# Kernel tuning notes

Measured on AMD Instinct MI355X. Metric: run time of the kernel, lower is better.

## Reference

```python
import jax, jax.numpy as jnp
import numpy as np

B, T, I, H, L, O = 256, 256, 128, 512, 2, 1


def _lstm_layer(x_tbi, W_ih, W_hh, b_ih, b_hh):
    # x_tbi: [T, B, in_dim]; returns full output sequence [T, B, H]
    # Precompute input projections for all timesteps at once (big GEMM).
    x_proj = jnp.einsum('tbi,gi->tbg', x_tbi, W_ih) + b_ih + b_hh  # [T, B, 4H]
    h0 = jnp.zeros((x_tbi.shape[1], H), x_tbi.dtype)
    c0 = jnp.zeros_like(h0)

    def step(carry, xp):
        h, c = carry
        gates = xp + h @ W_hh.T  # [B, 4H]
        i_g, f_g, g_g, o_g = jnp.split(gates, 4, axis=-1)  # torch order: i,f,g,o
        i_g = jax.nn.sigmoid(i_g)
        f_g = jax.nn.sigmoid(f_g)
        g_g = jnp.tanh(g_g)
        o_g = jax.nn.sigmoid(o_g)
        c_new = f_g * c + i_g * g_g
        h_new = o_g * jnp.tanh(c_new)
        return (h_new, c_new), h_new

    (_, _), hs = jax.lax.scan(step, (h0, c0), x_proj)
    return hs  # [T, B, H]


def setup_inputs() -> dict:
    key = jax.random.key(0)
    ks = jax.random.split(key, 11)
    s_ih0 = 1.0 / np.sqrt(H)
    inp = {
        'x': jax.random.normal(ks[0], (B, T, I), jnp.float32),
        'W_ih0': jax.random.uniform(ks[1], (4 * H, I), jnp.float32, -s_ih0, s_ih0),
        'W_hh0': jax.random.uniform(ks[2], (4 * H, H), jnp.float32, -s_ih0, s_ih0),
        'b_ih0': jax.random.uniform(ks[3], (4 * H,), jnp.float32, -s_ih0, s_ih0),
        'b_hh0': jax.random.uniform(ks[4], (4 * H,), jnp.float32, -s_ih0, s_ih0),
        'W_ih1': jax.random.uniform(ks[5], (4 * H, H), jnp.float32, -s_ih0, s_ih0),
        'W_hh1': jax.random.uniform(ks[6], (4 * H, H), jnp.float32, -s_ih0, s_ih0),
        'b_ih1': jax.random.uniform(ks[7], (4 * H,), jnp.float32, -s_ih0, s_ih0),
        'b_hh1': jax.random.uniform(ks[8], (4 * H,), jnp.float32, -s_ih0, s_ih0),
        'fc_w': jax.random.uniform(ks[9], (O, H), jnp.float32, -s_ih0, s_ih0),
        'fc_b': jax.random.uniform(ks[10], (O,), jnp.float32, -s_ih0, s_ih0),
    }
    return inp


def reference(x, W_ih0, W_hh0, b_ih0, b_hh0, W_ih1, W_hh1, b_ih1, b_hh1, fc_w, fc_b):
    x_tbi = jnp.transpose(x, (1, 0, 2))  # [T, B, I]
    h1 = _lstm_layer(x_tbi, W_ih0, W_hh0, b_ih0, b_hh0)  # [T, B, H]
    h2 = _lstm_layer(h1, W_ih1, W_hh1, b_ih1, b_hh1)     # [T, B, H]
    last = h2[-1]                                         # [B, H] == out[:, -1, :]
    return last @ fc_w.T + fc_b                           # [B, O]
```

## Files before the change

### kernel.cpp

```cpp
#include <hip/hip_runtime.h>
#include <stdint.h>

typedef _Float16 f16;
typedef _Float16 f16x8 __attribute__((ext_vector_type(8)));
typedef float f32x4 __attribute__((ext_vector_type(4)));

#define TT 256
#define BB 256
#define II 128
#define HH 512
#define G4 2048
#define NGRP 8
static constexpr size_t BH = (size_t)BB * HH;

__device__ __forceinline__ uint64_t ld_agent_u64(const uint64_t* p) {
  return __hip_atomic_load(p, __ATOMIC_RELAXED, __HIP_MEMORY_SCOPE_AGENT);
}
__device__ __forceinline__ void st_agent_u64(uint64_t* p, uint64_t v) {
  __hip_atomic_store(p, v, __ATOMIC_RELAXED, __HIP_MEMORY_SCOPE_AGENT);
}
__device__ __forceinline__ void st_agent_u16(uint16_t* p, uint16_t v) {
  __hip_atomic_store(p, v, __ATOMIC_RELAXED, __HIP_MEMORY_SCOPE_AGENT);
}
__device__ __forceinline__ uint4 mk4(uint64_t a, uint64_t b) {
  uint4 r;
  r.x = (uint32_t)a; r.y = (uint32_t)(a >> 32);
  r.z = (uint32_t)b; r.w = (uint32_t)(b >> 32);
  return r;
}

__device__ __forceinline__ float fsig(float x) {
  x = fminf(fmaxf(x, -30.f), 30.f);
  float e = __builtin_amdgcn_exp2f(-1.44269504f * x);
  return __builtin_amdgcn_rcpf(1.f + e);
}
__device__ __forceinline__ float ftanh(float x) {
  x = fminf(fmaxf(x, -15.f), 15.f);
  float e = __builtin_amdgcn_exp2f(-2.88539008f * x);
  return (1.f - e) * __builtin_amdgcn_rcpf(1.f + e);
}

__device__ __forceinline__ f16x8 ldfragh(const f16* S, int row, int gi) {
  return *(const f16x8*)(S + row * 512 + ((gi ^ (row & 7)) * 8));
}
__device__ __forceinline__ f16x8 ldfragx(const f16* S, int row, int gi) {
  return *(const f16x8*)(S + row * 128 + ((gi ^ (row & 7)) * 8));
}

__global__ void k_diag(float* out, float val) { out[0] = val; }

__global__ __launch_bounds__(256) void k_conv_x(const float* __restrict__ x,
                                                f16* __restrict__ xt) {
  int idx = blockIdx.x * 256 + threadIdx.x;
  int row = idx >> 4;
  int ii = (idx & 15) * 8;
  int t = row >> 8, b = row & 255;
  const float4* xs = (const float4*)(x + ((size_t)b * TT + t) * II + ii);
  float4 v0 = xs[0];
  float4 v1 = xs[1];
  f16x8 h;
  h[0] = (f16)v0.x; h[1] = (f16)v0.y; h[2] = (f16)v0.z; h[3] = (f16)v0.w;
  h[4] = (f16)v1.x; h[5] = (f16)v1.y; h[6] = (f16)v1.z; h[7] = (f16)v1.w;
  *(f16x8*)(xt + (size_t)row * II + ii) = h;
}

__global__ __launch_bounds__(256) void k_conv_w(
    const float* __restrict__ wih0, const float* __restrict__ whh0,
    const float* __restrict__ wih1, const float* __restrict__ whh1,
    const float* __restrict__ bih0, const float* __restrict__ bhh0,
    const float* __restrict__ bih1, const float* __restrict__ bhh1,
    f16* owih0, f16* owhh0, f16* owih1, f16* owhh1, float* ob0, float* ob1) {
  int i = blockIdx.x * 256 + threadIdx.x;
  if (i < G4 * II) owih0[i] = (f16)wih0[i];
  if (i < G4 * HH) {
    owhh0[i] = (f16)whh0[i];
    owih1[i] = (f16)wih1[i];
    owhh1[i] = (f16)whh1[i];
  }
  if (i < G4) {
    ob0[i] = bih0[i] + bhh0[i];
    ob1[i] = bih1[i] + bhh1[i];
  }
}

__global__ __launch_bounds__(256, 1) void k_fused(
    const f16* __restrict__ xt,
    const f16* __restrict__ Wih0, const f16* __restrict__ Whh0,
    const f16* __restrict__ Wih1, const f16* __restrict__ Whh1,
    const float* __restrict__ b0, const float* __restrict__ b1,
    f16* __restrict__ h1r, f16* __restrict__ h2r, uint16_t* __restrict__ flags) {
  __shared__ __align__(16) f16 h1s[32 * 512];
  __shared__ __align__(16) f16 h2s[32 * 512];
  __shared__ __align__(16) f16 xs[32 * 128];
  __shared__ __align__(16) float gs[2][64][36];

  int tid = threadIdx.x;
  int l64 = tid & 63;
  int wid = tid >> 6;
  int lm = l64 & 15, ls = l64 >> 4;
  int bx = blockIdx.x;
  int grp = bx & 7;
  int slice = bx >> 3;
  int col0 = slice * 16;
  int row0 = grp * 32;

  int wrow = wid * 512 + col0 + lm;
  f16x8 wih0f[4], whh0f[16], wih1f[16], whh1f[16];
#pragma unroll
  for (int kk = 0; kk < 4; ++kk)
    wih0f[kk] = *(const f16x8*)(Wih0 + (size_t)wrow * II + kk * 32 + ls * 8);
#pragma unroll
  for (int kk = 0; kk < 16; ++kk) {
    whh0f[kk] = *(const f16x8*)(Whh0 + (size_t)wrow * HH + kk * 32 + ls * 8);
    wih1f[kk] = *(const f16x8*)(Wih1 + (size_t)wrow * HH + kk * 32 + ls * 8);
    whh1f[kk] = *(const f16x8*)(Whh1 + (size_t)wrow * HH + kk * 32 + ls * 8);
  }

  int el = tid >> 7;
  int er = (tid >> 2) & 31;
  int eq = tid & 3;
  const float* bsrc = el ? b1 : b0;
  float bias[4][4];
#pragma unroll
  for (int g = 0; g < 4; ++g)
#pragma unroll
    for (int j = 0; j < 4; ++j) bias[g][j] = bsrc[g * HH + col0 + eq * 4 + j];
  float cst[4] = {0.f, 0.f, 0.f, 0.f};
  f16* ering = el ? h2r : h1r;

  int sr = tid >> 3;
  int gx = tid & 7;
  const uint64_t kTarget = 0x0001000100010001ULL;

#pragma unroll 1
  for (int u = 0; u <= TT; ++u) {
    uint4 xv0, xv1;
    if (u < TT) {
      const uint4* src = (const uint4*)(xt + ((size_t)u * BB + row0 + sr) * II);
      xv0 = src[gx];
      xv1 = src[gx + 8];
    }
    if (u > 0) {
      const uint64_t* fl =
          (const uint64_t*)(flags + ((size_t)grp * (TT + 1) + (u - 1)) * 32);
      int guard = 0;
      for (;;) {
        uint64_t v = ld_agent_u64(fl + (l64 & 3));
        if (__all(v == kTarget)) break;
        if (++guard > 200000) break;
        __builtin_amdgcn_s_sleep(1);
      }
      asm volatile("" ::: "memory");
      const uint64_t* s1 = (const uint64_t*)(h1r + (size_t)((u - 1) & 1) * BH +
                                             (size_t)(row0 + sr) * HH);
      uint64_t va[16], vb[16];
#pragma unroll
      for (int q = 0; q < 8; ++q) {
        int gi = gx + q * 8;
        va[2 * q]     = ld_agent_u64(s1 + gi * 2);
        va[2 * q + 1] = ld_agent_u64(s1 + gi * 2 + 1);
      }
      if (u >= 2) {
        const uint64_t* s2 = (const uint64_t*)(h2r + (size_t)(u & 1) * BH +
                                               (size_t)(row0 + sr) * HH);
#pragma unroll
        for (int q = 0; q < 8; ++q) {
          int gi = gx + q * 8;
          vb[2 * q]     = ld_agent_u64(s2 + gi * 2);
          vb[2 * q + 1] = ld_agent_u64(s2 + gi * 2 + 1);
        }
      }
      uint4* d1 = (uint4*)h1s;
#pragma unroll
      for (int q = 0; q < 8; ++q) {
        int gi = gx + q * 8;
        d1[sr * 64 + (gi ^ (sr & 7))] = mk4(va[2 * q], va[2 * q + 1]);
      }
      if (u >= 2) {
        uint4* d2 = (uint4*)h2s;
#pragma unroll
        for (int q = 0; q < 8; ++q) {
          int gi = gx + q * 8;
          d2[sr * 64 + (gi ^ (sr & 7))] = mk4(vb[2 * q], vb[2 * q + 1]);
        }
      }
    }
    if (u < TT) {
      uint4* dx = (uint4*)xs;
      dx[sr * 16 + (gx ^ (sr & 7))] = xv0;
      dx[sr * 16 + ((gx + 8) ^ (sr & 7))] = xv1;
    }
    __syncthreads();

    f32x4 a0f0 = {0.f, 0.f, 0.f, 0.f}, a0f1 = {0.f, 0.f, 0.f, 0.f};
    f32x4 a1f0 = {0.f, 0.f, 0.f, 0.f}, a1f1 = {0.f, 0.f, 0.f, 0.f};
    if (u < TT) {
#pragma unroll
      for (int kk = 0; kk < 4; ++kk) {
        f16x8 xA = ldfragx(xs, lm, kk * 4 + ls);
        f16x8 xB = ldfragx(xs, 16 + lm, kk * 4 + ls);
        a0f0 = __builtin_amdgcn_mfma_f32_16x16x32_f16(xA, wih0f[kk], a0f0, 0, 0, 0);
        a0f1 = __builtin_amdgcn_mfma_f32_16x16x32_f16(xB, wih0f[kk], a0f1, 0, 0, 0);
      }
    }
    if (u > 0) {
#pragma unroll
      for (int kk = 0; kk < 16; ++kk) {
        f16x8 hA = ldfragh(h1s, lm, kk * 4 + ls);
        f16x8 hB = ldfragh(h1s, 16 + lm, kk * 4 + ls);
        if (u < TT) {
          a0f0 = __builtin_amdgcn_mfma_f32_16x16x32_f16(hA, whh0f[kk], a0f0, 0, 0, 0);
          a0f1 = __builtin_amdgcn_mfma_f32_16x16x32_f16(hB, whh0f[kk], a0f1, 0, 0, 0);
        }
        a1f0 = __builtin_amdgcn_mfma_f32_16x16x32_f16(hA, wih1f[kk], a1f0, 0, 0, 0);
        a1f1 = __builtin_amdgcn_mfma_f32_16x16x32_f16(hB, wih1f[kk], a1f1, 0, 0, 0);
      }
      if (u >= 2) {
#pragma unroll
        for (int kk = 0; kk < 16; ++kk) {
          f16x8 hA = ldfragh(h2s, lm, kk * 4 + ls);
          f16x8 hB = ldfragh(h2s, 16 + lm, kk * 4 + ls);
          a1f0 = __builtin_amdgcn_mfma_f32_16x16x32_f16(hA, whh1f[kk], a1f0, 0, 0, 0);
          a1f1 = __builtin_amdgcn_mfma_f32_16x16x32_f16(hB, whh1f[kk], a1f1, 0, 0, 0);
        }
      }
    }
    *(f32x4*)&gs[0][wid * 16 + lm][ls * 4] = a0f0;
    *(f32x4*)&gs[0][wid * 16 + lm][16 + ls * 4] = a0f1;
    *(f32x4*)&gs[1][wid * 16 + lm][ls * 4] = a1f0;
    *(f32x4*)&gs[1][wid * 16 + lm][16 + ls * 4] = a1f1;
    __syncthreads();

    bool act = el ? (u >= 1) : (u < TT);
    if (act) {
      int t_l = el ? (u - 1) : u;
      int slot = t_l & 1;
      union { uint64_t v; unsigned short us[4]; } pk;
#pragma unroll
      for (int j = 0; j < 4; ++j) {
        int cl = eq * 4 + j;
        float pi = gs[el][0 * 16 + cl][er] + bias[0][j];
        float pf = gs[el][1 * 16 + cl][er] + bias[1][j];
        float pg = gs[el][2 * 16 + cl][er] + bias[2][j];
        float po = gs[el][3 * 16 + cl][er] + bias[3][j];
        float ig = fsig(pi), fg = fsig(pf), gg = ftanh(pg), og = fsig(po);
        cst[j] = fg * cst[j] + ig * gg;
        pk.us[j] = __builtin_bit_cast(unsigned short, (f16)(og * ftanh(cst[j])));
      }
      uint64_t* dst = (uint64_t*)(ering + (size_t)slot * BH +
                                  (size_t)(row0 + er) * HH + col0 + eq * 4);
      st_agent_u64(dst, pk.v);
    }
    asm volatile("s_waitcnt vmcnt(0)" ::: "memory");
    __syncthreads();
    if (u < TT && tid == 0)
      st_agent_u16(flags + ((size_t)grp * (TT + 1) + u) * 32 + slice, 1u);
  }
}

__global__ __launch_bounds__(64) void k_fc(const f16* __restrict__ h2,
                                           const float* __restrict__ fcw,
                                           const float* __restrict__ fcb,
                                           float* __restrict__ out) {
  int b = blockIdx.x;
  int l = threadIdx.x;
  f16x8 hv = *(const f16x8*)(h2 + (size_t)b * HH + l * 8);
  float4 w0 = ((const float4*)fcw)[l * 2];
  float4 w1 = ((const float4*)fcw)[l * 2 + 1];
  float s = (float)hv[0] * w0.x + (float)hv[1] * w0.y + (float)hv[2] * w0.z +
            (float)hv[3] * w0.w + (float)hv[4] * w1.x + (float)hv[5] * w1.y +
            (float)hv[6] * w1.z + (float)hv[7] * w1.w;
#pragma unroll
  for (int off = 32; off > 0; off >>= 1) s += __shfl_down(s, off);
  if (l == 0) out[b] = s + fcb[0];
}

extern "C" void kernel_launch(void* const* d_in, const int* in_sizes, int n_in,
                              void* d_out, int out_size, void* d_ws, size_t ws_size,
                              hipStream_t stream) {
  (void)in_sizes; (void)n_in; (void)out_size;

  const float* x    = (const float*)d_in[0];
  const float* wih0 = (const float*)d_in[1];
  const float* whh0 = (const float*)d_in[2];
  const float* bih0 = (const float*)d_in[3];
  const float* bhh0 = (const float*)d_in[4];
  const float* wih1 = (const float*)d_in[5];
  const float* whh1 = (const float*)d_in[6];
  const float* bih1 = (const float*)d_in[7];
  const float* bhh1 = (const float*)d_in[8];
  const float* fcw  = (const float*)d_in[9];
  const float* fcb  = (const float*)d_in[10];

  const size_t SZ_XT   = (size_t)TT * BB * II * 2;
  const size_t SZ_WIH0 = (size_t)G4 * II * 2;
  const size_t SZ_W    = (size_t)G4 * HH * 2;
  const size_t SZ_B    = (size_t)G4 * 4;
  const size_t SZ_RING = (size_t)2 * BH * 2;
  const size_t SZ_FLG  = (size_t)NGRP * (TT + 1) * 64;
  const size_t TOTAL = SZ_XT + SZ_WIH0 + 3 * SZ_W + 2 * SZ_B + 2 * SZ_RING + SZ_FLG;

  if (ws_size < TOTAL) {
    k_diag<<<1, 1, 0, stream>>>((float*)d_out, (float)(ws_size >> 20));
    return;
  }

  char* ws = (char*)d_ws;
  size_t off = 0;
  f16* xt    = (f16*)(ws + off); off += SZ_XT;
  f16* cwih0 = (f16*)(ws + off); off += SZ_WIH0;
  f16* cwhh0 = (f16*)(ws + off); off += SZ_W;
  f16* cwih1 = (f16*)(ws + off); off += SZ_W;
  f16* cwhh1 = (f16*)(ws + off); off += SZ_W;
  float* b0  = (float*)(ws + off); off += SZ_B;
  float* b1  = (float*)(ws + off); off += SZ_B;
  f16* h1r   = (f16*)(ws + off); off += SZ_RING;
  f16* h2r   = (f16*)(ws + off); off += SZ_RING;
  uint16_t* flags = (uint16_t*)(ws + off); off += SZ_FLG;

  hipMemsetAsync(flags, 0, SZ_FLG, stream);
  k_conv_w<<<4096, 256, 0, stream>>>(wih0, whh0, wih1, whh1, bih0, bhh0, bih1, bhh1,
                                     cwih0, cwhh0, cwih1, cwhh1, b0, b1);
  k_conv_x<<<4096, 256, 0, stream>>>(x, xt);
  k_fused<<<256, 256, 0, stream>>>(xt, cwih0, cwhh0, cwih1, cwhh1, b0, b1,
                                   h1r, h2r, flags);
  k_fc<<<256, 64, 0, stream>>>(h2r + BH, fcw, fcb, (float*)d_out);
}
```

Before: 1.559 ms.

## Halve persistent block count with 512-thread blocks covering 32 hidden columns each

The fused persistent LSTM kernel now launches 128 blocks of 512 threads instead of 256 blocks of 256. Each block covers 32 hidden columns with two waves per gate, which halves the number of blocks that must signal and poll flags every timestep. The h-state ring reload now uses inline-asm dwordx4 loads with the sc1 cache bit instead of 64-bit agent-scope atomic loads. Biases are staged in shared memory rather than held in registers. In exchange, per-step elementwise work per block doubles and more threads wait at each barrier, and the sc1 loads depend on that bit giving coherent reads of data written by other blocks.

```diff
diff --git a/kernel.cpp b/kernel.cpp
--- a/kernel.cpp
+++ b/kernel.cpp
@@ -11,6 +11,7 @@
 #define HH 512
 #define G4 2048
 #define NGRP 8
+#define NSLC 16
 static constexpr size_t BH = (size_t)BB * HH;
 
 __device__ __forceinline__ uint64_t ld_agent_u64(const uint64_t* p) {
@@ -22,11 +23,21 @@
 __device__ __forceinline__ void st_agent_u16(uint16_t* p, uint16_t v) {
   __hip_atomic_store(p, v, __ATOMIC_RELAXED, __HIP_MEMORY_SCOPE_AGENT);
 }
-__device__ __forceinline__ uint4 mk4(uint64_t a, uint64_t b) {
-  uint4 r;
-  r.x = (uint32_t)a; r.y = (uint32_t)(a >> 32);
-  r.z = (uint32_t)b; r.w = (uint32_t)(b >> 32);
-  return r;
+__device__ __forceinline__ void ld8_sc1(const void* b1, const void* b2, uint4 v[8]) {
+  asm volatile(
+      "global_load_dwordx4 %0, %8, off sc1\n\t"
+      "global_load_dwordx4 %1, %8, off offset:256 sc1\n\t"
+      "global_load_dwordx4 %2, %8, off offset:512 sc1\n\t"
+      "global_load_dwordx4 %3, %8, off offset:768 sc1\n\t"
+      "global_load_dwordx4 %4, %9, off sc1\n\t"
+      "global_load_dwordx4 %5, %9, off offset:256 sc1\n\t"
+      "global_load_dwordx4 %6, %9, off offset:512 sc1\n\t"
+      "global_load_dwordx4 %7, %9, off offset:768 sc1\n\t"
+      "s_waitcnt vmcnt(4)"
+      : "=&v"(v[0]), "=&v"(v[1]), "=&v"(v[2]), "=&v"(v[3]),
+        "=&v"(v[4]), "=&v"(v[5]), "=&v"(v[6]), "=&v"(v[7])
+      : "v"(b1), "v"(b2)
+      : "memory");
 }
 
 __device__ __forceinline__ float fsig(float x) {
@@ -83,7 +94,7 @@
   }
 }
 
-__global__ __launch_bounds__(256, 1) void k_fused(
+__global__ __launch_bounds__(512, 2) void k_fused(
     const f16* __restrict__ xt,
     const f16* __restrict__ Wih0, const f16* __restrict__ Whh0,
     const f16* __restrict__ Wih1, const f16* __restrict__ Whh1,
@@ -92,19 +103,28 @@
   __shared__ __align__(16) f16 h1s[32 * 512];
   __shared__ __align__(16) f16 h2s[32 * 512];
   __shared__ __align__(16) f16 xs[32 * 128];
-  __shared__ __align__(16) float gs[2][64][36];
+  __shared__ __align__(16) float gs[2][128][36];
+  __shared__ float bl[2][4][32];
 
   int tid = threadIdx.x;
   int l64 = tid & 63;
   int wid = tid >> 6;
+  int g = wid >> 1;
+  int ch = wid & 1;
   int lm = l64 & 15, ls = l64 >> 4;
   int bx = blockIdx.x;
   int grp = bx & 7;
   int slice = bx >> 3;
-  int col0 = slice * 16;
+  int col0 = slice * 32;
   int row0 = grp * 32;
 
-  int wrow = wid * 512 + col0 + lm;
+  if (tid < 256) {
+    int el_ = tid >> 7, gt = (tid >> 5) & 3, cl = tid & 31;
+    const float* bsrc = el_ ? b1 : b0;
+    bl[el_][gt][cl] = bsrc[gt * HH + col0 + cl];
+  }
+
+  int wrow = g * 512 + col0 + ch * 16 + lm;
   f16x8 wih0f[4], whh0f[16], wih1f[16], whh1f[16];
 #pragma unroll
   for (int kk = 0; kk < 4; ++kk)
@@ -116,79 +136,55 @@
     whh1f[kk] = *(const f16x8*)(Whh1 + (size_t)wrow * HH + kk * 32 + ls * 8);
   }
 
-  int el = tid >> 7;
-  int er = (tid >> 2) & 31;
-  int eq = tid & 3;
-  const float* bsrc = el ? b1 : b0;
-  float bias[4][4];
-#pragma unroll
-  for (int g = 0; g < 4; ++g)
-#pragma unroll
-    for (int j = 0; j < 4; ++j) bias[g][j] = bsrc[g * HH + col0 + eq * 4 + j];
+  int el = tid >> 8;
+  int er = (tid >> 3) & 31;
+  int eq = tid & 7;
   float cst[4] = {0.f, 0.f, 0.f, 0.f};
   f16* ering = el ? h2r : h1r;
 
-  int sr = tid >> 3;
-  int gx = tid & 7;
+  int sr = tid >> 4;
+  int gq = tid & 15;
   const uint64_t kTarget = 0x0001000100010001ULL;
+  __syncthreads();
 
 #pragma unroll 1
   for (int u = 0; u <= TT; ++u) {
-    uint4 xv0, xv1;
-    if (u < TT) {
-      const uint4* src = (const uint4*)(xt + ((size_t)u * BB + row0 + sr) * II);
-      xv0 = src[gx];
-      xv1 = src[gx + 8];
-    }
+    uint4 xv;
+    if (u < TT)
+      xv = ((const uint4*)(xt + ((size_t)u * BB + row0 + sr) * II))[gq];
     if (u > 0) {
       const uint64_t* fl =
           (const uint64_t*)(flags + ((size_t)grp * (TT + 1) + (u - 1)) * 32);
       int guard = 0;
       for (;;) {
-        uint64_t v = ld_agent_u64(fl + (l64 & 3));
+        uint64_t v = ld_agent_u64(fl + (l64 & 1));
         if (__all(v == kTarget)) break;
-        if (++guard > 200000) break;
+        if (++guard > 500000) break;
         __builtin_amdgcn_s_sleep(1);
       }
       asm volatile("" ::: "memory");
-      const uint64_t* s1 = (const uint64_t*)(h1r + (size_t)((u - 1) & 1) * BH +
-                                             (size_t)(row0 + sr) * HH);
-      uint64_t va[16], vb[16];
-#pragma unroll
-      for (int q = 0; q < 8; ++q) {
-        int gi = gx + q * 8;
-        va[2 * q]     = ld_agent_u64(s1 + gi * 2);
-        va[2 * q + 1] = ld_agent_u64(s1 + gi * 2 + 1);
-      }
-      if (u >= 2) {
-        const uint64_t* s2 = (const uint64_t*)(h2r + (size_t)(u & 1) * BH +
-                                               (size_t)(row0 + sr) * HH);
-#pragma unroll
-        for (int q = 0; q < 8; ++q) {
-          int gi = gx + q * 8;
-          vb[2 * q]     = ld_agent_u64(s2 + gi * 2);
-          vb[2 * q + 1] = ld_agent_u64(s2 + gi * 2 + 1);
-        }
-      }
+      const f16* base1 =
+          h1r + (size_t)((u - 1) & 1) * BH + (size_t)(row0 + sr) * HH + gq * 8;
+      const f16* base2 =
+          h2r + (size_t)(u & 1) * BH + (size_t)(row0 + sr) * HH + gq * 8;
+      uint4 v[8];
+      ld8_sc1(base1, base2, v);
       uint4* d1 = (uint4*)h1s;
-#pragma unroll
-      for (int q = 0; q < 8; ++q) {
-        int gi = gx + q * 8;
-        d1[sr * 64 + (gi ^ (sr & 7))] = mk4(va[2 * q], va[2 * q + 1]);
-      }
-      if (u >= 2) {
-        uint4* d2 = (uint4*)h2s;
-#pragma unroll
-        for (int q = 0; q < 8; ++q) {
-          int gi = gx + q * 8;
-          d2[sr * 64 + (gi ^ (sr & 7))] = mk4(vb[2 * q], vb[2 * q + 1]);
-        }
+      uint4* d2 = (uint4*)h2s;
+#pragma unroll
+      for (int q = 0; q < 4; ++q) {
+        int gi = gq + q * 16;
+        d1[sr * 64 + (gi ^ (sr & 7))] = v[q];
+      }
+      asm volatile("s_waitcnt vmcnt(0)" ::: "memory");
+#pragma unroll
+      for (int q = 0; q < 4; ++q) {
+        int gi = gq + q * 16;
+        d2[sr * 64 + (gi ^ (sr & 7))] = v[4 + q];
       }
     }
     if (u < TT) {
-      uint4* dx = (uint4*)xs;
-      dx[sr * 16 + (gx ^ (sr & 7))] = xv0;
-      dx[sr * 16 + ((gx + 8) ^ (sr & 7))] = xv1;
+      ((uint4*)xs)[sr * 16 + (gq ^ (sr & 7))] = xv;
     }
     __syncthreads();
 
@@ -225,10 +221,11 @@
         }
       }
     }
-    *(f32x4*)&gs[0][wid * 16 + lm][ls * 4] = a0f0;
-    *(f32x4*)&gs[0][wid * 16 + lm][16 + ls * 4] = a0f1;
-    *(f32x4*)&gs[1][wid * 16 + lm][ls * 4] = a1f0;
-    *(f32x4*)&gs[1][wid * 16 + lm][16 + ls * 4] = a1f1;
+    int gl = g * 32 + ch * 16 + lm;
+    *(f32x4*)&gs[0][gl][ls * 4] = a0f0;
+    *(f32x4*)&gs[0][gl][16 + ls * 4] = a0f1;
+    *(f32x4*)&gs[1][gl][ls * 4] = a1f0;
+    *(f32x4*)&gs[1][gl][16 + ls * 4] = a1f1;
     __syncthreads();
 
     bool act = el ? (u >= 1) : (u < TT);
@@ -239,10 +236,10 @@
 #pragma unroll
       for (int j = 0; j < 4; ++j) {
         int cl = eq * 4 + j;
-        float pi = gs[el][0 * 16 + cl][er] + bias[0][j];
-        float pf = gs[el][1 * 16 + cl][er] + bias[1][j];
-        float pg = gs[el][2 * 16 + cl][er] + bias[2][j];
-        float po = gs[el][3 * 16 + cl][er] + bias[3][j];
+        float pi = gs[el][0 * 32 + cl][er] + bl[el][0][cl];
+        float pf = gs[el][1 * 32 + cl][er] + bl[el][1][cl];
+        float pg = gs[el][2 * 32 + cl][er] + bl[el][2][cl];
+        float po = gs[el][3 * 32 + cl][er] + bl[el][3][cl];
         float ig = fsig(pi), fg = fsig(pf), gg = ftanh(pg), og = fsig(po);
         cst[j] = fg * cst[j] + ig * gg;
         pk.us[j] = __builtin_bit_cast(unsigned short, (f16)(og * ftanh(cst[j])));
@@ -298,7 +295,8 @@
   const size_t SZ_B    = (size_t)G4 * 4;
   const size_t SZ_RING = (size_t)2 * BH * 2;
   const size_t SZ_FLG  = (size_t)NGRP * (TT + 1) * 64;
-  const size_t TOTAL = SZ_XT + SZ_WIH0 + 3 * SZ_W + 2 * SZ_B + 2 * SZ_RING + SZ_FLG;
+  const size_t TOTAL =
+      SZ_XT + SZ_WIH0 + 3 * SZ_W + 2 * SZ_B + 2 * SZ_RING + SZ_FLG;
 
   if (ws_size < TOTAL) {
     k_diag<<<1, 1, 0, stream>>>((float*)d_out, (float)(ws_size >> 20));
@@ -322,7 +320,7 @@
   k_conv_w<<<4096, 256, 0, stream>>>(wih0, whh0, wih1, whh1, bih0, bhh0, bih1, bhh1,
                                      cwih0, cwhh0, cwih1, cwhh1, b0, b1);
   k_conv_x<<<4096, 256, 0, stream>>>(x, xt);
-  k_fused<<<256, 256, 0, stream>>>(xt, cwih0, cwhh0, cwih1, cwhh1, b0, b1,
+  k_fused<<<128, 512, 0, stream>>>(xt, cwih0, cwhh0, cwih1, cwhh1, b0, b1,
                                    h1r, h2r, flags);
   k_fc<<<256, 64, 0, stream>>>(h2r + BH, fcw, fcb, (float*)d_out);
 }
```

Result: slower. 1.866 ms (+19.7%).

## Split per-layer flags and publish layer-0 h before layer-1 GEMM

Applied to the files above, without the earlier changes.

Gives each layer its own flag array and per-wave flag lanes, so layer-0 hidden state is computed, stored and signalled right after the layer-0 GEMM, before the layer-1 GEMM runs. This moves layer 0 off the critical path of layer 1 and lets other blocks start the next step earlier. The h1/h2 ring reads become one batch of inline-asm dwordx4 loads with the sc1 cache bit, and the h2 LDS write is deferred until after the layer-0 MFMAs. This adds an extra barrier per step, hand-written waitcnt logic, and a wait on both layers' flags.

```diff
diff --git a/kernel.cpp b/kernel.cpp
--- a/kernel.cpp
+++ b/kernel.cpp
@@ -12,6 +12,8 @@
 #define G4 2048
 #define NGRP 8
 static constexpr size_t BH = (size_t)BB * HH;
+static constexpr size_t FLG_LINE_U16 = 64;
+static constexpr size_t FLG_LAYER_OFF = (size_t)NGRP * (TT + 1) * FLG_LINE_U16;
 
 __device__ __forceinline__ uint64_t ld_agent_u64(const uint64_t* p) {
   return __hip_atomic_load(p, __ATOMIC_RELAXED, __HIP_MEMORY_SCOPE_AGENT);
@@ -22,11 +24,31 @@
 __device__ __forceinline__ void st_agent_u16(uint16_t* p, uint16_t v) {
   __hip_atomic_store(p, v, __ATOMIC_RELAXED, __HIP_MEMORY_SCOPE_AGENT);
 }
-__device__ __forceinline__ uint4 mk4(uint64_t a, uint64_t b) {
-  uint4 r;
-  r.x = (uint32_t)a; r.y = (uint32_t)(a >> 32);
-  r.z = (uint32_t)b; r.w = (uint32_t)(b >> 32);
-  return r;
+__device__ __forceinline__ void ld16_sc1(const void* b1, const void* b2, uint4 v[16]) {
+  asm volatile(
+      "global_load_dwordx4 %0, %16, off sc1\n\t"
+      "global_load_dwordx4 %1, %16, off offset:128 sc1\n\t"
+      "global_load_dwordx4 %2, %16, off offset:256 sc1\n\t"
+      "global_load_dwordx4 %3, %16, off offset:384 sc1\n\t"
+      "global_load_dwordx4 %4, %16, off offset:512 sc1\n\t"
+      "global_load_dwordx4 %5, %16, off offset:640 sc1\n\t"
+      "global_load_dwordx4 %6, %16, off offset:768 sc1\n\t"
+      "global_load_dwordx4 %7, %16, off offset:896 sc1\n\t"
+      "global_load_dwordx4 %8, %17, off sc1\n\t"
+      "global_load_dwordx4 %9, %17, off offset:128 sc1\n\t"
+      "global_load_dwordx4 %10, %17, off offset:256 sc1\n\t"
+      "global_load_dwordx4 %11, %17, off offset:384 sc1\n\t"
+      "global_load_dwordx4 %12, %17, off offset:512 sc1\n\t"
+      "global_load_dwordx4 %13, %17, off offset:640 sc1\n\t"
+      "global_load_dwordx4 %14, %17, off offset:768 sc1\n\t"
+      "global_load_dwordx4 %15, %17, off offset:896 sc1\n\t"
+      "s_waitcnt vmcnt(8)"
+      : "=&v"(v[0]), "=&v"(v[1]), "=&v"(v[2]), "=&v"(v[3]),
+        "=&v"(v[4]), "=&v"(v[5]), "=&v"(v[6]), "=&v"(v[7]),
+        "=&v"(v[8]), "=&v"(v[9]), "=&v"(v[10]), "=&v"(v[11]),
+        "=&v"(v[12]), "=&v"(v[13]), "=&v"(v[14]), "=&v"(v[15])
+      : "v"(b1), "v"(b2)
+      : "memory");
 }
 
 __device__ __forceinline__ float fsig(float x) {
@@ -140,49 +162,41 @@
       xv0 = src[gx];
       xv1 = src[gx + 8];
     }
+    uint4 hv[16];
     if (u > 0) {
-      const uint64_t* fl =
-          (const uint64_t*)(flags + ((size_t)grp * (TT + 1) + (u - 1)) * 32);
+      const uint64_t* fl1 =
+          (const uint64_t*)(flags + ((size_t)grp * (TT + 1) + (u - 1)) * FLG_LINE_U16);
+      const uint64_t* fl2 =
+          (const uint64_t*)(flags + FLG_LAYER_OFF +
+                            ((size_t)grp * (TT + 1) + (u >= 2 ? u - 2 : 0)) * FLG_LINE_U16);
       int guard = 0;
-      for (;;) {
-        uint64_t v = ld_agent_u64(fl + (l64 & 3));
-        if (__all(v == kTarget)) break;
-        if (++guard > 200000) break;
-        __builtin_amdgcn_s_sleep(1);
+      if (u >= 2) {
+        for (;;) {
+          uint64_t v1 = ld_agent_u64(fl1 + (l64 & 7));
+          uint64_t v2 = ld_agent_u64(fl2 + (l64 & 7));
+          if (__all((v1 == kTarget) && (v2 == kTarget))) break;
+          if (++guard > 500000) break;
+          __builtin_amdgcn_s_sleep(1);
+        }
+      } else {
+        for (;;) {
+          uint64_t v1 = ld_agent_u64(fl1 + (l64 & 7));
+          if (__all(v1 == kTarget)) break;
+          if (++guard > 500000) break;
+          __builtin_amdgcn_s_sleep(1);
+        }
       }
       asm volatile("" ::: "memory");
-      const uint64_t* s1 = (const uint64_t*)(h1r + (size_t)((u - 1) & 1) * BH +
-                                             (size_t)(row0 + sr) * HH);
-      uint64_t va[16], vb[16];
+      const f16* base1 =
+          h1r + (size_t)((u - 1) & 1) * BH + (size_t)(row0 + sr) * HH + gx * 8;
+      const f16* base2 =
+          h2r + (size_t)(u & 1) * BH + (size_t)(row0 + sr) * HH + gx * 8;
+      ld16_sc1(base1, base2, hv);
+      uint4* d1 = (uint4*)h1s;
 #pragma unroll
       for (int q = 0; q < 8; ++q) {
         int gi = gx + q * 8;
-        va[2 * q]     = ld_agent_u64(s1 + gi * 2);
-        va[2 * q + 1] = ld_agent_u64(s1 + gi * 2 + 1);
-      }
-      if (u >= 2) {
-        const uint64_t* s2 = (const uint64_t*)(h2r + (size_t)(u & 1) * BH +
-                                               (size_t)(row0 + sr) * HH);
-#pragma unroll
-        for (int q = 0; q < 8; ++q) {
-          int gi = gx + q * 8;
-          vb[2 * q]     = ld_agent_u64(s2 + gi * 2);
-          vb[2 * q + 1] = ld_agent_u64(s2 + gi * 2 + 1);
-        }
-      }
-      uint4* d1 = (uint4*)h1s;
-#pragma unroll
-      for (int q = 0; q < 8; ++q) {
-        int gi = gx + q * 8;
-        d1[sr * 64 + (gi ^ (sr & 7))] = mk4(va[2 * q], va[2 * q + 1]);
-      }
-      if (u >= 2) {
-        uint4* d2 = (uint4*)h2s;
-#pragma unroll
-        for (int q = 0; q < 8; ++q) {
-          int gi = gx + q * 8;
-          d2[sr * 64 + (gi ^ (sr & 7))] = mk4(vb[2 * q], vb[2 * q + 1]);
-        }
+        d1[sr * 64 + (gi ^ (sr & 7))] = hv[q];
       }
     }
     if (u < TT) {
@@ -192,9 +206,8 @@
     }
     __syncthreads();
 
-    f32x4 a0f0 = {0.f, 0.f, 0.f, 0.f}, a0f1 = {0.f, 0.f, 0.f, 0.f};
-    f32x4 a1f0 = {0.f, 0.f, 0.f, 0.f}, a1f1 = {0.f, 0.f, 0.f, 0.f};
     if (u < TT) {
+      f32x4 a0f0 = {0.f, 0.f, 0.f, 0.f}, a0f1 = {0.f, 0.f, 0.f, 0.f};
 #pragma unroll
       for (int kk = 0; kk < 4; ++kk) {
         f16x8 xA = ldfragx(xs, lm, kk * 4 + ls);
@@ -202,16 +215,58 @@
         a0f0 = __builtin_amdgcn_mfma_f32_16x16x32_f16(xA, wih0f[kk], a0f0, 0, 0, 0);
         a0f1 = __builtin_amdgcn_mfma_f32_16x16x32_f16(xB, wih0f[kk], a0f1, 0, 0, 0);
       }
+      if (u > 0) {
+#pragma unroll
+        for (int kk = 0; kk < 16; ++kk) {
+          f16x8 hA = ldfragh(h1s, lm, kk * 4 + ls);
+          f16x8 hB = ldfragh(h1s, 16 + lm, kk * 4 + ls);
+          a0f0 = __builtin_amdgcn_mfma_f32_16x16x32_f16(hA, whh0f[kk], a0f0, 0, 0, 0);
+          a0f1 = __builtin_amdgcn_mfma_f32_16x16x32_f16(hB, whh0f[kk], a0f1, 0, 0, 0);
+        }
+      }
+      *(f32x4*)&gs[0][wid * 16 + lm][ls * 4] = a0f0;
+      *(f32x4*)&gs[0][wid * 16 + lm][16 + ls * 4] = a0f1;
     }
     if (u > 0) {
+      asm volatile("s_waitcnt vmcnt(0)" ::: "memory");
+      uint4* d2 = (uint4*)h2s;
+#pragma unroll
+      for (int q = 0; q < 8; ++q) {
+        int gi = gx + q * 8;
+        d2[sr * 64 + (gi ^ (sr & 7))] = hv[8 + q];
+      }
+    }
+    __syncthreads();
+
+    if (u < TT && wid < 2) {
+      union { uint64_t v; unsigned short us[4]; } pk;
+#pragma unroll
+      for (int j = 0; j < 4; ++j) {
+        int cl = eq * 4 + j;
+        float pi = gs[0][0 * 16 + cl][er] + bias[0][j];
+        float pf = gs[0][1 * 16 + cl][er] + bias[1][j];
+        float pg = gs[0][2 * 16 + cl][er] + bias[2][j];
+        float po = gs[0][3 * 16 + cl][er] + bias[3][j];
+        float ig = fsig(pi), fg = fsig(pf), gg = ftanh(pg), og = fsig(po);
+        cst[j] = fg * cst[j] + ig * gg;
+        pk.us[j] = __builtin_bit_cast(unsigned short, (f16)(og * ftanh(cst[j])));
+      }
+      st_agent_u64((uint64_t*)(h1r + (size_t)(u & 1) * BH +
+                               (size_t)(row0 + er) * HH + col0 + eq * 4),
+                   pk.v);
+      asm volatile("s_waitcnt vmcnt(0)" ::: "memory");
+      if (l64 == 0)
+        st_agent_u16(flags + ((size_t)grp * (TT + 1) + u) * FLG_LINE_U16 +
+                         slice * 2 + wid,
+                     1u);
+    }
+
+    if (u > 0) {
+      f32x4 a1f0 = {0.f, 0.f, 0.f, 0.f}, a1f1 = {0.f, 0.f, 0.f, 0.f};
 #pragma unroll
       for (int kk = 0; kk < 16; ++kk) {
         f16x8 hA = ldfragh(h1s, lm, kk * 4 + ls);
         f16x8 hB = ldfragh(h1s, 16 + lm, kk * 4 + ls);
-        if (u < TT) {
-          a0f0 = __builtin_amdgcn_mfma_f32_16x16x32_f16(hA, whh0f[kk], a0f0, 0, 0, 0);
-          a0f1 = __builtin_amdgcn_mfma_f32_16x16x32_f16(hB, whh0f[kk], a0f1, 0, 0, 0);
-        }
         a1f0 = __builtin_amdgcn_mfma_f32_16x16x32_f16(hA, wih1f[kk], a1f0, 0, 0, 0);
         a1f1 = __builtin_amdgcn_mfma_f32_16x16x32_f16(hB, wih1f[kk], a1f1, 0, 0, 0);
       }
@@ -224,37 +279,34 @@
           a1f1 = __builtin_amdgcn_mfma_f32_16x16x32_f16(hB, whh1f[kk], a1f1, 0, 0, 0);
         }
       }
-    }
-    *(f32x4*)&gs[0][wid * 16 + lm][ls * 4] = a0f0;
-    *(f32x4*)&gs[0][wid * 16 + lm][16 + ls * 4] = a0f1;
-    *(f32x4*)&gs[1][wid * 16 + lm][ls * 4] = a1f0;
-    *(f32x4*)&gs[1][wid * 16 + lm][16 + ls * 4] = a1f1;
+      *(f32x4*)&gs[1][wid * 16 + lm][ls * 4] = a1f0;
+      *(f32x4*)&gs[1][wid * 16 + lm][16 + ls * 4] = a1f1;
+    }
     __syncthreads();
 
-    bool act = el ? (u >= 1) : (u < TT);
-    if (act) {
-      int t_l = el ? (u - 1) : u;
-      int slot = t_l & 1;
+    if (u > 0 && wid >= 2) {
       union { uint64_t v; unsigned short us[4]; } pk;
 #pragma unroll
       for (int j = 0; j < 4; ++j) {
         int cl = eq * 4 + j;
-        float pi = gs[el][0 * 16 + cl][er] + bias[0][j];
-        float pf = gs[el][1 * 16 + cl][er] + bias[1][j];
-        float pg = gs[el][2 * 16 + cl][er] + bias[2][j];
-        float po = gs[el][3 * 16 + cl][er] + bias[3][j];
+        float pi = gs[1][0 * 16 + cl][er] + bias[0][j];
+        float pf = gs[1][1 * 16 + cl][er] + bias[1][j];
+        float pg = gs[1][2 * 16 + cl][er] + bias[2][j];
+        float po = gs[1][3 * 16 + cl][er] + bias[3][j];
         float ig = fsig(pi), fg = fsig(pf), gg = ftanh(pg), og = fsig(po);
         cst[j] = fg * cst[j] + ig * gg;
         pk.us[j] = __builtin_bit_cast(unsigned short, (f16)(og * ftanh(cst[j])));
       }
-      uint64_t* dst = (uint64_t*)(ering + (size_t)slot * BH +
-                                  (size_t)(row0 + er) * HH + col0 + eq * 4);
-      st_agent_u64(dst, pk.v);
-    }
-    asm volatile("s_waitcnt vmcnt(0)" ::: "memory");
-    __syncthreads();
-    if (u < TT && tid == 0)
-      st_agent_u16(flags + ((size_t)grp * (TT + 1) + u) * 32 + slice, 1u);
+      st_agent_u64((uint64_t*)(h2r + (size_t)((u - 1) & 1) * BH +
+                               (size_t)(row0 + er) * HH + col0 + eq * 4),
+                   pk.v);
+      asm volatile("s_waitcnt vmcnt(0)" ::: "memory");
+      if (l64 == 0)
+        st_agent_u16(flags + FLG_LAYER_OFF +
+                         ((size_t)grp * (TT + 1) + (u - 1)) * FLG_LINE_U16 +
+                         slice * 2 + (wid - 2),
+                     1u);
+    }
   }
 }
 
@@ -297,8 +349,9 @@
   const size_t SZ_W    = (size_t)G4 * HH * 2;
   const size_t SZ_B    = (size_t)G4 * 4;
   const size_t SZ_RING = (size_t)2 * BH * 2;
-  const size_t SZ_FLG  = (size_t)NGRP * (TT + 1) * 64;
-  const size_t TOTAL = SZ_XT + SZ_WIH0 + 3 * SZ_W + 2 * SZ_B + 2 * SZ_RING + SZ_FLG;
+  const size_t SZ_FLG  = (size_t)2 * NGRP * (TT + 1) * FLG_LINE_U16 * 2;
+  const size_t TOTAL =
+      SZ_XT + SZ_WIH0 + 3 * SZ_W + 2 * SZ_B + 2 * SZ_RING + SZ_FLG;
 
   if (ws_size < TOTAL) {
     k_diag<<<1, 1, 0, stream>>>((float*)d_out, (float)(ws_size >> 20));
```

New measurement: 2.129 ms. 36.6% more time.

## Split layers into separate producer/consumer blocks with per-wave flags and 4-slot ring

Applied to the files above, without the earlier changes.

Splits the persistent fused kernel into two block roles, one running layer 0 and one running layer 1, and launches twice as many blocks. Layer 1 consumes layer-0 outputs through a 4-slot ring, so layer 0 can run up to three steps ahead, and each role keeps only its own weights in registers. Flags are now per-wave on separate cache lines, so the end-of-step block barrier is gone. Hidden-state loads use inline-asm dwordx4 loads with sc1. The risks are the extra cross-block synchronisation per step for layer 1, deadlock if both roles are not co-resident, and the guard-bounded spin loops.

```diff
diff --git a/kernel.cpp b/kernel.cpp
--- a/kernel.cpp
+++ b/kernel.cpp
@@ -12,21 +12,33 @@
 #define G4 2048
 #define NGRP 8
 static constexpr size_t BH = (size_t)BB * HH;
+static constexpr size_t FLG_LINE_U16 = 128;
+static constexpr size_t FLG_ARR_U16 = (size_t)NGRP * (TT + 1) * FLG_LINE_U16;
 
 __device__ __forceinline__ uint64_t ld_agent_u64(const uint64_t* p) {
   return __hip_atomic_load(p, __ATOMIC_RELAXED, __HIP_MEMORY_SCOPE_AGENT);
 }
-__device__ __forceinline__ void st_agent_u64(uint64_t* p, uint64_t v) {
+__device__ __forceinline__ void st_agent_u32(uint32_t* p, uint32_t v) {
   __hip_atomic_store(p, v, __ATOMIC_RELAXED, __HIP_MEMORY_SCOPE_AGENT);
 }
 __device__ __forceinline__ void st_agent_u16(uint16_t* p, uint16_t v) {
   __hip_atomic_store(p, v, __ATOMIC_RELAXED, __HIP_MEMORY_SCOPE_AGENT);
 }
-__device__ __forceinline__ uint4 mk4(uint64_t a, uint64_t b) {
-  uint4 r;
-  r.x = (uint32_t)a; r.y = (uint32_t)(a >> 32);
-  r.z = (uint32_t)b; r.w = (uint32_t)(b >> 32);
-  return r;
+__device__ __forceinline__ void ld8t_sc1(const void* b, uint4 v[8]) {
+  asm volatile(
+      "global_load_dwordx4 %0, %8, off sc1\n\t"
+      "global_load_dwordx4 %1, %8, off offset:128 sc1\n\t"
+      "global_load_dwordx4 %2, %8, off offset:256 sc1\n\t"
+      "global_load_dwordx4 %3, %8, off offset:384 sc1\n\t"
+      "global_load_dwordx4 %4, %8, off offset:512 sc1\n\t"
+      "global_load_dwordx4 %5, %8, off offset:640 sc1\n\t"
+      "global_load_dwordx4 %6, %8, off offset:768 sc1\n\t"
+      "global_load_dwordx4 %7, %8, off offset:896 sc1\n\t"
+      "s_waitcnt vmcnt(0)"
+      : "=&v"(v[0]), "=&v"(v[1]), "=&v"(v[2]), "=&v"(v[3]),
+        "=&v"(v[4]), "=&v"(v[5]), "=&v"(v[6]), "=&v"(v[7])
+      : "v"(b)
+      : "memory");
 }
 
 __device__ __forceinline__ float fsig(float x) {
@@ -83,178 +95,244 @@
   }
 }
 
-__global__ __launch_bounds__(256, 1) void k_fused(
+__global__ __launch_bounds__(256, 2) void k_fused(
     const f16* __restrict__ xt,
     const f16* __restrict__ Wih0, const f16* __restrict__ Whh0,
     const f16* __restrict__ Wih1, const f16* __restrict__ Whh1,
     const float* __restrict__ b0, const float* __restrict__ b1,
-    f16* __restrict__ h1r, f16* __restrict__ h2r, uint16_t* __restrict__ flags) {
+    f16* __restrict__ h1r, f16* __restrict__ h2r,
+    uint16_t* __restrict__ flag1, uint16_t* __restrict__ flagL1) {
   __shared__ __align__(16) f16 h1s[32 * 512];
   __shared__ __align__(16) f16 h2s[32 * 512];
-  __shared__ __align__(16) f16 xs[32 * 128];
-  __shared__ __align__(16) float gs[2][64][36];
+  __shared__ __align__(16) float gs[64][36];
 
   int tid = threadIdx.x;
   int l64 = tid & 63;
   int wid = tid >> 6;
   int lm = l64 & 15, ls = l64 >> 4;
   int bx = blockIdx.x;
-  int grp = bx & 7;
-  int slice = bx >> 3;
+  int role = bx & 1;
+  int id = bx >> 1;
+  int grp = id & 7;
+  int slice = id >> 3;
   int col0 = slice * 16;
   int row0 = grp * 32;
-
-  int wrow = wid * 512 + col0 + lm;
-  f16x8 wih0f[4], whh0f[16], wih1f[16], whh1f[16];
-#pragma unroll
-  for (int kk = 0; kk < 4; ++kk)
-    wih0f[kk] = *(const f16x8*)(Wih0 + (size_t)wrow * II + kk * 32 + ls * 8);
-#pragma unroll
-  for (int kk = 0; kk < 16; ++kk) {
-    whh0f[kk] = *(const f16x8*)(Whh0 + (size_t)wrow * HH + kk * 32 + ls * 8);
-    wih1f[kk] = *(const f16x8*)(Wih1 + (size_t)wrow * HH + kk * 32 + ls * 8);
-    whh1f[kk] = *(const f16x8*)(Whh1 + (size_t)wrow * HH + kk * 32 + ls * 8);
-  }
-
-  int el = tid >> 7;
-  int er = (tid >> 2) & 31;
-  int eq = tid & 3;
-  const float* bsrc = el ? b1 : b0;
-  float bias[4][4];
-#pragma unroll
-  for (int g = 0; g < 4; ++g)
-#pragma unroll
-    for (int j = 0; j < 4; ++j) bias[g][j] = bsrc[g * HH + col0 + eq * 4 + j];
-  float cst[4] = {0.f, 0.f, 0.f, 0.f};
-  f16* ering = el ? h2r : h1r;
-
   int sr = tid >> 3;
   int gx = tid & 7;
-  const uint64_t kTarget = 0x0001000100010001ULL;
+  int er = tid >> 3;
+  int eq = tid & 7;
+  const uint64_t kT = 0x0001000100010001ULL;
+
+  if (role == 0) {
+    int wrow = wid * 512 + col0 + lm;
+    f16x8 wi[4], wh[16];
+#pragma unroll
+    for (int kk = 0; kk < 4; ++kk)
+      wi[kk] = *(const f16x8*)(Wih0 + (size_t)wrow * II + kk * 32 + ls * 8);
+#pragma unroll
+    for (int kk = 0; kk < 16; ++kk)
+      wh[kk] = *(const f16x8*)(Whh0 + (size_t)wrow * HH + kk * 32 + ls * 8);
+    float bias[4][2];
+#pragma unroll
+    for (int g = 0; g < 4; ++g)
+#pragma unroll
+      for (int j = 0; j < 2; ++j) bias[g][j] = b0[g * HH + col0 + eq * 2 + j];
+    float c1[2] = {0.f, 0.f};
+    f16* xs = (f16*)h2s;
 
 #pragma unroll 1
-  for (int u = 0; u <= TT; ++u) {
-    uint4 xv0, xv1;
-    if (u < TT) {
-      const uint4* src = (const uint4*)(xt + ((size_t)u * BB + row0 + sr) * II);
-      xv0 = src[gx];
-      xv1 = src[gx + 8];
-    }
-    if (u > 0) {
-      const uint64_t* fl =
-          (const uint64_t*)(flags + ((size_t)grp * (TT + 1) + (u - 1)) * 32);
-      int guard = 0;
-      for (;;) {
-        uint64_t v = ld_agent_u64(fl + (l64 & 3));
-        if (__all(v == kTarget)) break;
-        if (++guard > 200000) break;
-        __builtin_amdgcn_s_sleep(1);
-      }
-      asm volatile("" ::: "memory");
-      const uint64_t* s1 = (const uint64_t*)(h1r + (size_t)((u - 1) & 1) * BH +
-                                             (size_t)(row0 + sr) * HH);
-      uint64_t va[16], vb[16];
-#pragma unroll
-      for (int q = 0; q < 8; ++q) {
-        int gi = gx + q * 8;
-        va[2 * q]     = ld_agent_u64(s1 + gi * 2);
-        va[2 * q + 1] = ld_agent_u64(s1 + gi * 2 + 1);
-      }
-      if (u >= 2) {
-        const uint64_t* s2 = (const uint64_t*)(h2r + (size_t)(u & 1) * BH +
-                                               (size_t)(row0 + sr) * HH);
+    for (int u = 0; u < TT; ++u) {
+      {
+        const uint4* src = (const uint4*)(xt + ((size_t)u * BB + row0 + sr) * II);
+        uint4 xv0 = src[gx];
+        uint4 xv1 = src[gx + 8];
+        uint4* dx = (uint4*)xs;
+        dx[sr * 16 + (gx ^ (sr & 7))] = xv0;
+        dx[sr * 16 + ((gx + 8) ^ (sr & 7))] = xv1;
+      }
+      if (u > 0) {
+        const uint64_t* f1 =
+            (const uint64_t*)(flag1 + ((size_t)grp * (TT + 1) + (u - 1)) * FLG_LINE_U16);
+        const uint64_t* f2 =
+            (const uint64_t*)(flagL1 +
+                              ((size_t)grp * (TT + 1) + (u >= 4 ? u - 4 : 0)) * FLG_LINE_U16);
+        int guard = 0;
+        for (;;) {
+          uint64_t v1 = ld_agent_u64(f1 + (l64 & 31));
+          bool ok = (v1 == kT);
+          if (u >= 4) {
+            uint64_t v2 = ld_agent_u64(f2 + (l64 & 31));
+            ok = ok && (v2 == kT);
+          }
+          if (__all(ok)) break;
+          if (++guard > 800000) break;
+          __builtin_amdgcn_s_sleep(1);
+        }
+        asm volatile("" ::: "memory");
+        const f16* base =
+            h1r + (size_t)((u - 1) & 3) * BH + (size_t)(row0 + sr) * HH + gx * 8;
+        uint4 hv[8];
+        ld8t_sc1(base, hv);
+        uint4* d1 = (uint4*)h1s;
 #pragma unroll
         for (int q = 0; q < 8; ++q) {
           int gi = gx + q * 8;
-          vb[2 * q]     = ld_agent_u64(s2 + gi * 2);
-          vb[2 * q + 1] = ld_agent_u64(s2 + gi * 2 + 1);
-        }
-      }
-      uint4* d1 = (uint4*)h1s;
-#pragma unroll
-      for (int q = 0; q < 8; ++q) {
-        int gi = gx + q * 8;
-        d1[sr * 64 + (gi ^ (sr & 7))] = mk4(va[2 * q], va[2 * q + 1]);
-      }
-      if (u >= 2) {
-        uint4* d2 = (uint4*)h2s;
-#pragma unroll
-        for (int q = 0; q < 8; ++q) {
-          int gi = gx + q * 8;
-          d2[sr * 64 + (gi ^ (sr & 7))] = mk4(vb[2 * q], vb[2 * q + 1]);
-        }
-      }
-    }
-    if (u < TT) {
-      uint4* dx = (uint4*)xs;
-      dx[sr * 16 + (gx ^ (sr & 7))] = xv0;
-      dx[sr * 16 + ((gx + 8) ^ (sr & 7))] = xv1;
-    }
-    __syncthreads();
-
-    f32x4 a0f0 = {0.f, 0.f, 0.f, 0.f}, a0f1 = {0.f, 0.f, 0.f, 0.f};
-    f32x4 a1f0 = {0.f, 0.f, 0.f, 0.f}, a1f1 = {0.f, 0.f, 0.f, 0.f};
-    if (u < TT) {
+          d1[sr * 64 + (gi ^ (sr & 7))] = hv[q];
+        }
+      }
+      __syncthreads();
+
+      f32x4 a0 = {0.f, 0.f, 0.f, 0.f}, a1 = {0.f, 0.f, 0.f, 0.f};
 #pragma unroll
       for (int kk = 0; kk < 4; ++kk) {
         f16x8 xA = ldfragx(xs, lm, kk * 4 + ls);
         f16x8 xB = ldfragx(xs, 16 + lm, kk * 4 + ls);
-        a0f0 = __builtin_amdgcn_mfma_f32_16x16x32_f16(xA, wih0f[kk], a0f0, 0, 0, 0);
-        a0f1 = __builtin_amdgcn_mfma_f32_16x16x32_f16(xB, wih0f[kk], a0f1, 0, 0, 0);
-      }
+        a0 = __builtin_amdgcn_mfma_f32_16x16x32_f16(xA, wi[kk], a0, 0, 0, 0);
+        a1 = __builtin_amdgcn_mfma_f32_16x16x32_f16(xB, wi[kk], a1, 0, 0, 0);
+      }
+      if (u > 0) {
+#pragma unroll
+        for (int kk = 0; kk < 16; ++kk) {
+          f16x8 hA = ldfragh(h1s, lm, kk * 4 + ls);
+          f16x8 hB = ldfragh(h1s, 16 + lm, kk * 4 + ls);
+          a0 = __builtin_amdgcn_mfma_f32_16x16x32_f16(hA, wh[kk], a0, 0, 0, 0);
+          a1 = __builtin_amdgcn_mfma_f32_16x16x32_f16(hB, wh[kk], a1, 0, 0, 0);
+        }
+      }
+      *(f32x4*)&gs[wid * 16 + lm][ls * 4] = a0;
+      *(f32x4*)&gs[wid * 16 + lm][16 + ls * 4] = a1;
+      __syncthreads();
+
+      union { uint32_t v; unsigned short us[2]; } pk;
+#pragma unroll
+      for (int j = 0; j < 2; ++j) {
+        int cl = eq * 2 + j;
+        float pi = gs[0 * 16 + cl][er] + bias[0][j];
+        float pf = gs[1 * 16 + cl][er] + bias[1][j];
+        float pg = gs[2 * 16 + cl][er] + bias[2][j];
+        float po = gs[3 * 16 + cl][er] + bias[3][j];
+        float ig = fsig(pi), fg = fsig(pf), gg = ftanh(pg), og = fsig(po);
+        c1[j] = fg * c1[j] + ig * gg;
+        pk.us[j] = __builtin_bit_cast(unsigned short, (f16)(og * ftanh(c1[j])));
+      }
+      st_agent_u32((uint32_t*)(h1r + (size_t)(u & 3) * BH +
+                               (size_t)(row0 + er) * HH + col0 + eq * 2),
+                   pk.v);
+      asm volatile("s_waitcnt vmcnt(0)" ::: "memory");
+      if (l64 == 0)
+        st_agent_u16(flag1 + ((size_t)grp * (TT + 1) + u) * FLG_LINE_U16 +
+                         slice * 4 + wid,
+                     1u);
     }
-    if (u > 0) {
+  } else {
+    int wrow = wid * 512 + col0 + lm;
+    f16x8 wi[16], wh[16];
+#pragma unroll
+    for (int kk = 0; kk < 16; ++kk) {
+      wi[kk] = *(const f16x8*)(Wih1 + (size_t)wrow * HH + kk * 32 + ls * 8);
+      wh[kk] = *(const f16x8*)(Whh1 + (size_t)wrow * HH + kk * 32 + ls * 8);
+    }
+    float bias[4][2];
+#pragma unroll
+    for (int g = 0; g < 4; ++g)
+#pragma unroll
+      for (int j = 0; j < 2; ++j) bias[g][j] = b1[g * HH + col0 + eq * 2 + j];
+    float c2[2] = {0.f, 0.f};
+
+#pragma unroll 1
+    for (int v = 0; v < TT; ++v) {
+      {
+        const uint64_t* f1 =
+            (const uint64_t*)(flag1 + ((size_t)grp * (TT + 1) + v) * FLG_LINE_U16);
+        int guard = 0;
+        for (;;) {
+          uint64_t v1 = ld_agent_u64(f1 + (l64 & 31));
+          if (__all(v1 == kT)) break;
+          if (++guard > 800000) break;
+          __builtin_amdgcn_s_sleep(1);
+        }
+        asm volatile("" ::: "memory");
+      }
+      {
+        const f16* base =
+            h1r + (size_t)(v & 3) * BH + (size_t)(row0 + sr) * HH + gx * 8;
+        uint4 hv[8];
+        ld8t_sc1(base, hv);
+        uint4* d1 = (uint4*)h1s;
+#pragma unroll
+        for (int q = 0; q < 8; ++q) {
+          int gi = gx + q * 8;
+          d1[sr * 64 + (gi ^ (sr & 7))] = hv[q];
+        }
+      }
+      __syncthreads();
+
+      f32x4 a0 = {0.f, 0.f, 0.f, 0.f}, a1 = {0.f, 0.f, 0.f, 0.f};
 #pragma unroll
       for (int kk = 0; kk < 16; ++kk) {
         f16x8 hA = ldfragh(h1s, lm, kk * 4 + ls);
         f16x8 hB = ldfragh(h1s, 16 + lm, kk * 4 + ls);
-        if (u < TT) {
-          a0f0 = __builtin_amdgcn_mfma_f32_16x16x32_f16(hA, whh0f[kk], a0f0, 0, 0, 0);
-          a0f1 = __builtin_amdgcn_mfma_f32_16x16x32_f16(hB, whh0f[kk], a0f1, 0, 0, 0);
-        }
-        a1f0 = __builtin_amdgcn_mfma_f32_16x16x32_f16(hA, wih1f[kk], a1f0, 0, 0, 0);
-        a1f1 = __builtin_amdgcn_mfma_f32_16x16x32_f16(hB, wih1f[kk], a1f1, 0, 0, 0);
-      }
-      if (u >= 2) {
+        a0 = __builtin_amdgcn_mfma_f32_16x16x32_f16(hA, wi[kk], a0, 0, 0, 0);
+        a1 = __builtin_amdgcn_mfma_f32_16x16x32_f16(hB, wi[kk], a1, 0, 0, 0);
+      }
+      if (v > 0) {
+        const uint64_t* f2 =
+            (const uint64_t*)(flagL1 + ((size_t)grp * (TT + 1) + (v - 1)) * FLG_LINE_U16);
+        int guard = 0;
+        for (;;) {
+          uint64_t v2 = ld_agent_u64(f2 + (l64 & 31));
+          if (__all(v2 == kT)) break;
+          if (++guard > 800000) break;
+          __builtin_amdgcn_s_sleep(1);
+        }
+        asm volatile("" ::: "memory");
+        const f16* base =
+            h2r + (size_t)((v - 1) & 1) * BH + (size_t)(row0 + sr) * HH + gx * 8;
+        uint4 hv[8];
+        ld8t_sc1(base, hv);
+        uint4* d2 = (uint4*)h2s;
+#pragma unroll
+        for (int q = 0; q < 8; ++q) {
+          int gi = gx + q * 8;
+          d2[sr * 64 + (gi ^ (sr & 7))] = hv[q];
+        }
+      }
+      __syncthreads();
+
+      if (v > 0) {
 #pragma unroll
         for (int kk = 0; kk < 16; ++kk) {
-          f16x8 hA = ldfragh(h2s, lm, kk * 4 + ls);
-          f16x8 hB = ldfragh(h2s, 16 + lm, kk * 4 + ls);
-          a1f0 = __builtin_amdgcn_mfma_f32_16x16x32_f16(hA, whh1f[kk], a1f0, 0, 0, 0);
-          a1f1 = __builtin_amdgcn_mfma_f32_16x16x32_f16(hB, whh1f[kk], a1f1, 0, 0, 0);
-        }
-      }
+          f16x8 kA = ldfragh(h2s, lm, kk * 4 + ls);
+          f16x8 kB = ldfragh(h2s, 16 + lm, kk * 4 + ls);
+          a0 = __builtin_amdgcn_mfma_f32_16x16x32_f16(kA, wh[kk], a0, 0, 0, 0);
+          a1 = __builtin_amdgcn_mfma_f32_16x16x32_f16(kB, wh[kk], a1, 0, 0, 0);
+        }
+      }
+      *(f32x4*)&gs[wid * 16 + lm][ls * 4] = a0;
+      *(f32x4*)&gs[wid * 16 + lm][16 + ls * 4] = a1;
+      __syncthreads();
+
+      union { uint32_t v; unsigned short us[2]; } pk;
+#pragma unroll
+      for (int j = 0; j < 2; ++j) {
+        int cl = eq * 2 + j;
+        float pi = gs[0 * 16 + cl][er] + bias[0][j];
+        float pf = gs[1 * 16 + cl][er] + bias[1][j];
+        float pg = gs[2 * 16 + cl][er] + bias[2][j];
+        float po = gs[3 * 16 + cl][er] + bias[3][j];
+        float ig = fsig(pi), fg = fsig(pf), gg = ftanh(pg), og = fsig(po);
+        c2[j] = fg * c2[j] + ig * gg;
+        pk.us[j] = __builtin_bit_cast(unsigned short, (f16)(og * ftanh(c2[j])));
+      }
+      st_agent_u32((uint32_t*)(h2r + (size_t)(v & 1) * BH +
+                               (size_t)(row0 + er) * HH + col0 + eq * 2),
+                   pk.v);
+      asm volatile("s_waitcnt vmcnt(0)" ::: "memory");
+      if (l64 == 0)
+        st_agent_u16(flagL1 + ((size_t)grp * (TT + 1) + v) * FLG_LINE_U16 +
+                         slice * 4 + wid,
+                     1u);
     }
-    *(f32x4*)&gs[0][wid * 16 + lm][ls * 4] = a0f0;
-    *(f32x4*)&gs[0][wid * 16 + lm][16 + ls * 4] = a0f1;
-    *(f32x4*)&gs[1][wid * 16 + lm][ls * 4] = a1f0;
-    *(f32x4*)&gs[1][wid * 16 + lm][16 + ls * 4] = a1f1;
-    __syncthreads();
-
-    bool act = el ? (u >= 1) : (u < TT);
-    if (act) {
-      int t_l = el ? (u - 1) : u;
-      int slot = t_l & 1;
-      union { uint64_t v; unsigned short us[4]; } pk;
-#pragma unroll
-      for (int j = 0; j < 4; ++j) {
-        int cl = eq * 4 + j;
-        float pi = gs[el][0 * 16 + cl][er] + bias[0][j];
-        float pf = gs[el][1 * 16 + cl][er] + bias[1][j];
-        float pg = gs[el][2 * 16 + cl][er] + bias[2][j];
-        float po = gs[el][3 * 16 + cl][er] + bias[3][j];
-        float ig = fsig(pi), fg = fsig(pf), gg = ftanh(pg), og = fsig(po);
-        cst[j] = fg * cst[j] + ig * gg;
-        pk.us[j] = __builtin_bit_cast(unsigned short, (f16)(og * ftanh(cst[j])));
-      }
-      uint64_t* dst = (uint64_t*)(ering + (size_t)slot * BH +
-                                  (size_t)(row0 + er) * HH + col0 + eq * 4);
-      st_agent_u64(dst, pk.v);
-    }
-    asm volatile("s_waitcnt vmcnt(0)" ::: "memory");
-    __syncthreads();
-    if (u < TT && tid == 0)
-      st_agent_u16(flags + ((size_t)grp * (TT + 1) + u) * 32 + slice, 1u);
   }
 }
 
@@ -292,13 +370,15 @@
   const float* fcw  = (const float*)d_in[9];
   const float* fcb  = (const float*)d_in[10];
 
-  const size_t SZ_XT   = (size_t)TT * BB * II * 2;
-  const size_t SZ_WIH0 = (size_t)G4 * II * 2;
-  const size_t SZ_W    = (size_t)G4 * HH * 2;
-  const size_t SZ_B    = (size_t)G4 * 4;
-  const size_t SZ_RING = (size_t)2 * BH * 2;
-  const size_t SZ_FLG  = (size_t)NGRP * (TT + 1) * 64;
-  const size_t TOTAL = SZ_XT + SZ_WIH0 + 3 * SZ_W + 2 * SZ_B + 2 * SZ_RING + SZ_FLG;
+  const size_t SZ_XT    = (size_t)TT * BB * II * 2;
+  const size_t SZ_WIH0  = (size_t)G4 * II * 2;
+  const size_t SZ_W     = (size_t)G4 * HH * 2;
+  const size_t SZ_B     = (size_t)G4 * 4;
+  const size_t SZ_RING1 = (size_t)4 * BH * 2;
+  const size_t SZ_RING2 = (size_t)2 * BH * 2;
+  const size_t SZ_FLG   = FLG_ARR_U16 * 2 * 2;
+  const size_t TOTAL = SZ_XT + SZ_WIH0 + 3 * SZ_W + 2 * SZ_B + SZ_RING1 +
+                       SZ_RING2 + SZ_FLG;
 
   if (ws_size < TOTAL) {
     k_diag<<<1, 1, 0, stream>>>((float*)d_out, (float)(ws_size >> 20));
@@ -314,15 +394,16 @@
   f16* cwhh1 = (f16*)(ws + off); off += SZ_W;
   float* b0  = (float*)(ws + off); off += SZ_B;
   float* b1  = (float*)(ws + off); off += SZ_B;
-  f16* h1r   = (f16*)(ws + off); off += SZ_RING;
-  f16* h2r   = (f16*)(ws + off); off += SZ_RING;
-  uint16_t* flags = (uint16_t*)(ws + off); off += SZ_FLG;
-
-  hipMemsetAsync(flags, 0, SZ_FLG, stream);
+  f16* h1r   = (f16*)(ws + off); off += SZ_RING1;
+  f16* h2r   = (f16*)(ws + off); off += SZ_RING2;
+  uint16_t* flag1  = (uint16_t*)(ws + off); off += FLG_ARR_U16 * 2;
+  uint16_t* flagL1 = (uint16_t*)(ws + off); off += FLG_ARR_U16 * 2;
+
+  hipMemsetAsync(flag1, 0, SZ_FLG, stream);
   k_conv_w<<<4096, 256, 0, stream>>>(wih0, whh0, wih1, whh1, bih0, bhh0, bih1, bhh1,
                                      cwih0, cwhh0, cwih1, cwhh1, b0, b1);
   k_conv_x<<<4096, 256, 0, stream>>>(x, xt);
-  k_fused<<<256, 256, 0, stream>>>(xt, cwih0, cwhh0, cwih1, cwhh1, b0, b1,
-                                   h1r, h2r, flags);
+  k_fused<<<512, 256, 0, stream>>>(xt, cwih0, cwhh0, cwih1, cwhh1, b0, b1,
+                                   h1r, h2r, flag1, flagL1);
   k_fc<<<256, 64, 0, stream>>>(h2r + BH, fcw, fcb, (float*)d_out);
 }
```

Measured after the change: 1.687 ms. 1.08x slower.
